# Kernel optimization log

Hardware: AMD Instinct MI355X
Metric: run time of the kernel (lower is better)

The kernel has to match this reference:

```python
import jax, jax.numpy as jnp
import numpy as np

B, NIN, DIN, M, DOUT = 256, 64, 128, 32, 128
SCALE = 1.0 / np.sqrt(DOUT)  # 1/sqrt(out_d_capsules)


def setup_inputs() -> dict:
    key = jax.random.key(0)
    k1, k2, k3 = jax.random.split(key, 3)
    w_const = float(np.sqrt(M / (DIN * NIN)))  # weight_init_const
    return {
        "x": jax.random.normal(k1, (B, NIN, DIN), dtype=jnp.float32),
        "current_act": jax.random.uniform(k2, (B, NIN), dtype=jnp.float32),
        "W": w_const * jax.random.normal(k3, (NIN, DIN, M, DOUT), dtype=jnp.float32),
        "num_iter": 3,
    }


def reference(x, current_act, W, num_iter):
    # Initial pass: next_capsule_value is None -> q0 = softmax(zeros) = 1/M uniform
    # einsum('nm,bna,namd->bmd', q0, x, W) with uniform q0 == mean over m-weighting = /M
    ncv = jnp.einsum('bna,namd->bmd', x, W) / M  # [B, M, Dout]
    q = jnp.full((B, NIN, M), 1.0 / M, dtype=x.dtype)  # query_key from init step
    # Routing iterations (act_type='EM' -> next_act is None; dp=0 -> no dropout)
    for _ in range(max(1, num_iter)):
        logits = jnp.einsum('bna,namd,bmd->bnm', x, W, ncv) * SCALE  # [B, Nin, M]
        q = jax.nn.softmax(logits, axis=2)
        ncv = jnp.einsum('bnm,bna,namd,bn->bmd', q, x, W, current_act)
    # Per-pair votes and routed class embeddings
    votes = jnp.einsum('bna,namd->bnmd', x, W)          # [B, Nin, M, Dout]
    weights = q * current_act[:, :, None]               # [B, Nin, M]
    route_class_emb = weights[..., None] * votes        # [B, Nin, M, Dout]
    return ncv, q, route_class_emb
```

## Files before the change

kernel.cpp:

```cpp
#include <hip/hip_runtime.h>
#include <math.h>

#define B_    256
#define NIN_  64
#define DIN_  128
#define M_    32
#define DOUT_ 128
#define NUM_ITER 3

static constexpr float SCALE = 0.0883883476483184405501f;

typedef __attribute__((ext_vector_type(8))) short bf16x8;
typedef __attribute__((ext_vector_type(4))) float f32x4;

__device__ __forceinline__ unsigned short f2bf(float f) {
    union { float f; unsigned u; } c; c.f = f;
    unsigned r = c.u + 0x7FFFu + ((c.u >> 16) & 1u);
    return (unsigned short)(r >> 16);
}
__device__ __forceinline__ float lo2f(unsigned u) {
    union { unsigned u; float f; } c; c.u = u << 16; return c.f;
}
__device__ __forceinline__ float hi2f(unsigned u) {
    union { unsigned u; float f; } c; c.u = u & 0xffff0000u; return c.f;
}


__global__ __launch_bounds__(256) void k_votes_mfma(const float* __restrict__ x,
                                                    const float* __restrict__ W,
                                                    float* __restrict__ route) {
    const int n    = blockIdx.x;
    const int j0   = blockIdx.y * 512;
    const int t    = threadIdx.x;
    const int w    = t >> 6;
    const int lane = t & 63;
    const int l15  = lane & 15;
    const int l4   = lane >> 4;

    __shared__ __align__(16) char lds[49152];
    char* xbuf = lds;
    char* wbuf = lds + 32768;

    bf16x8 af[4][4];

    for (int h = 0; h < 2; ++h) {
        {
            const int col4 = (t & 15) * 4;
            const int roff = t >> 4;
            const int boff = col4 * 2;
            for (int p = 0; p < 16; ++p) {
                int row = p * 16 + roff;
                const float* src = x + (size_t)row * (NIN_ * DIN_) + (size_t)n * DIN_ + h * 64 + col4;
                float4 v = *(const float4*)src;
                uint2 pk;
                pk.x = (unsigned)f2bf(v.x) | ((unsigned)f2bf(v.y) << 16);
                pk.y = (unsigned)f2bf(v.z) | ((unsigned)f2bf(v.w) << 16);
                *(uint2*)(xbuf + row * 128 + (boff ^ ((row & 7) << 4))) = pk;
            }
        }
        __syncthreads();
#pragma unroll
        for (int mf = 0; mf < 4; ++mf) {
            int row = w * 64 + mf * 16 + l15;
            int sw  = (row & 7) << 4;
#pragma unroll
            for (int kfh = 0; kfh < 2; ++kfh) {
                int kbyte = kfh * 64 + l4 * 16;
                af[mf][h * 2 + kfh] = *(const bf16x8*)(xbuf + row * 128 + (kbyte ^ sw));
            }
        }
        __syncthreads();
    }

    const int jlane = t & 63;
    const int kg    = t >> 6;

    for (int jt = 0; jt < 8; ++jt) {
        {
            const int jcol = j0 + jt * 64 + jlane;
            const float* Wp = W + (size_t)n * (DIN_ * M_ * DOUT_) + jcol;
            const int sw = (jlane & 7) << 4;
#pragma unroll
            for (int c = 0; c < 4; ++c) {
                int kbase = kg * 32 + c * 8;
                unsigned pk[4];
#pragma unroll
                for (int r = 0; r < 4; ++r) {
                    float f0 = __builtin_nontemporal_load(&Wp[(size_t)(kbase + 2 * r)     * 4096]);
                    float f1 = __builtin_nontemporal_load(&Wp[(size_t)(kbase + 2 * r + 1) * 4096]);
                    pk[r] = (unsigned)f2bf(f0) | ((unsigned)f2bf(f1) << 16);
                }
                *(uint4*)(wbuf + jlane * 256 + ((kbase * 2) ^ sw)) = *(uint4*)pk;
            }
        }
        __syncthreads();

        f32x4 acc[4][4];
#pragma unroll
        for (int mf = 0; mf < 4; ++mf)
#pragma unroll
            for (int nf = 0; nf < 4; ++nf) acc[mf][nf] = (f32x4){0.f, 0.f, 0.f, 0.f};

#pragma unroll
        for (int kf = 0; kf < 4; ++kf) {
            bf16x8 bfr[4];
            int kbyte = kf * 64 + l4 * 16;
#pragma unroll
            for (int nf = 0; nf < 4; ++nf) {
                int col = nf * 16 + l15;
                bfr[nf] = *(const bf16x8*)(wbuf + col * 256 + (kbyte ^ ((col & 7) << 4)));
            }
#pragma unroll
            for (int mf = 0; mf < 4; ++mf)
#pragma unroll
                for (int nf = 0; nf < 4; ++nf)
                    acc[mf][nf] = __builtin_amdgcn_mfma_f32_16x16x32_bf16(af[mf][kf], bfr[nf], acc[mf][nf], 0, 0, 0);
        }
        __syncthreads();

#pragma unroll
        for (int mf = 0; mf < 4; ++mf) {
#pragma unroll
            for (int nf = 0; nf < 4; ++nf) {
                const int jb = nf * 16 + l15;
#pragma unroll
                for (int r = 0; r < 4; ++r) {
                    const int b = w * 64 + mf * 16 + l4 * 4 + r;
                    *(unsigned short*)(xbuf + b * 128 + ((jb * 2) ^ ((b & 12) << 3))) = f2bf(acc[mf][nf][r]);
                }
            }
        }
        __syncthreads();

        {
            char* vout = (char*)route;
            const size_t obase = (size_t)524288 + (size_t)n * 8192 + (size_t)(j0 + jt * 64) * 2;
#pragma unroll
            for (int p = 0; p < 8; ++p) {
                const int b = p * 32 + (t >> 3);
                const int c = (t & 7) * 16;
                uint4 val = *(const uint4*)(xbuf + b * 128 + (c ^ ((b & 12) << 3)));
                *(uint4*)(vout + (size_t)b * 1048576 + obase + c) = val;
            }
        }
        __syncthreads();
    }
}

__global__ __launch_bounds__(512, 2) void k_fused(float* __restrict__ route,
                                                  const float* __restrict__ act,
                                                  float* __restrict__ ncv,
                                                  float* __restrict__ q_out) {
    const int b    = blockIdx.x;
    const int t    = threadIdx.x;
    const int base = t * 8;
    const int m    = t >> 4;

    __shared__ float logits_s[8][32];
    __shared__ float w_s[8][32];
    __shared__ float sact[NIN_];
    if (t < 64) sact[t] = act[b * 64 + t];

    const char* vb    = (const char*)route + (size_t)b * 1048576 + 524288;
    const size_t toff = (size_t)t * 16;

    uint4 vA[8], vB[8];
    float ncvp[8], acc[8];

#define LOADC(DST, CC) { \
    _Pragma("unroll") \
    for (int r = 0; r < 8; ++r) \
        DST[r] = *(const uint4*)(vb + (size_t)((CC) * 8 + r) * 8192 + toff); }

#define SUM8(V) { \
    _Pragma("unroll") \
    for (int r = 0; r < 8; ++r) { \
        acc[0] += lo2f(V[r].x); acc[1] += hi2f(V[r].x); \
        acc[2] += lo2f(V[r].y); acc[3] += hi2f(V[r].y); \
        acc[4] += lo2f(V[r].z); acc[5] += hi2f(V[r].z); \
        acc[6] += lo2f(V[r].w); acc[7] += hi2f(V[r].w); } }

#define PH_A(V) { \
    _Pragma("unroll") \
    for (int r = 0; r < 8; ++r) { \
        float p = 0.f; \
        p = fmaf(lo2f(V[r].x), ncvp[0], p); p = fmaf(hi2f(V[r].x), ncvp[1], p); \
        p = fmaf(lo2f(V[r].y), ncvp[2], p); p = fmaf(hi2f(V[r].y), ncvp[3], p); \
        p = fmaf(lo2f(V[r].z), ncvp[4], p); p = fmaf(hi2f(V[r].z), ncvp[5], p); \
        p = fmaf(lo2f(V[r].w), ncvp[6], p); p = fmaf(hi2f(V[r].w), ncvp[7], p); \
        p += __shfl_xor(p, 1); p += __shfl_xor(p, 2); \
        p += __shfl_xor(p, 4); p += __shfl_xor(p, 8); \
        if ((t & 15) == 0) logits_s[r][m] = p * SCALE; \
    } }

#define PH_B(CC, WRF) { \
    if (t < 256) { \
        const int rr = t >> 5; const int ln = t & 31; \
        float l  = logits_s[rr][ln]; \
        float mx = l; \
        mx = fmaxf(mx, __shfl_xor(mx, 1));  mx = fmaxf(mx, __shfl_xor(mx, 2)); \
        mx = fmaxf(mx, __shfl_xor(mx, 4));  mx = fmaxf(mx, __shfl_xor(mx, 8)); \
        mx = fmaxf(mx, __shfl_xor(mx, 16)); \
        float e  = __expf(l - mx); \
        float su = e; \
        su += __shfl_xor(su, 1);  su += __shfl_xor(su, 2); \
        su += __shfl_xor(su, 4);  su += __shfl_xor(su, 8);  su += __shfl_xor(su, 16); \
        float qv = e / su; \
        const int ng = (CC) * 8 + rr; \
        w_s[rr][ln] = qv * sact[ng]; \
        if (WRF) __builtin_nontemporal_store(qv, q_out + (size_t)b * 2048 + (size_t)ng * 32 + ln); \
    } }

#define PH_C(V, CC, WRF) { \
    _Pragma("unroll") \
    for (int r = 0; r < 8; ++r) { \
        const float wg = w_s[r][m]; \
        float f0 = lo2f(V[r].x), f1 = hi2f(V[r].x), f2 = lo2f(V[r].y), f3 = hi2f(V[r].y); \
        float f4 = lo2f(V[r].z), f5 = hi2f(V[r].z), f6 = lo2f(V[r].w), f7 = hi2f(V[r].w); \
        acc[0] = fmaf(wg, f0, acc[0]); acc[1] = fmaf(wg, f1, acc[1]); \
        acc[2] = fmaf(wg, f2, acc[2]); acc[3] = fmaf(wg, f3, acc[3]); \
        acc[4] = fmaf(wg, f4, acc[4]); acc[5] = fmaf(wg, f5, acc[5]); \
        acc[6] = fmaf(wg, f6, acc[6]); acc[7] = fmaf(wg, f7, acc[7]); \
        if (WRF) { \
            f32x4 r0 = {wg * f0, wg * f1, wg * f2, wg * f3}; \
            f32x4 r1 = {wg * f4, wg * f5, wg * f6, wg * f7}; \
            float* rp = route + (size_t)b * 262144 + (size_t)((CC) * 8 + r) * 4096 + base; \
            __builtin_nontemporal_store(r0, (f32x4*)rp); \
            __builtin_nontemporal_store(r1, (f32x4*)(rp + 4)); \
        } \
    } }

#define PROC(V, CC, WRF) { PH_A(V); __syncthreads(); PH_B(CC, WRF); __syncthreads(); PH_C(V, CC, WRF); }

#define ITER_PASS(WRF, WRAP) { \
    _Pragma("unroll") for (int i = 0; i < 8; ++i) acc[i] = 0.f; \
    LOADC(vB, 1); \
    for (int cc = 0; cc < 8; cc += 2) { \
        PROC(vA, cc, WRF); \
        if (cc + 2 < 8) { LOADC(vA, cc + 2); } \
        else if (WRAP)  { LOADC(vA, 0); } \
        PROC(vB, cc + 1, WRF); \
        if (cc + 3 < 8) { LOADC(vB, cc + 3); } \
    } \
    _Pragma("unroll") for (int i = 0; i < 8; ++i) ncvp[i] = acc[i]; }

#pragma unroll
    for (int i = 0; i < 8; ++i) acc[i] = 0.f;
    LOADC(vA, 0);
    LOADC(vB, 1);
    for (int cc = 0; cc < 8; cc += 2) {
        SUM8(vA);
        if (cc + 2 < 8) { LOADC(vA, cc + 2); }
        else            { LOADC(vA, 0); }
        SUM8(vB);
        if (cc + 3 < 8) { LOADC(vB, cc + 3); }
    }
#pragma unroll
    for (int i = 0; i < 8; ++i) ncvp[i] = acc[i] * (1.0f / 32.0f);

    for (int it = 0; it < NUM_ITER - 1; ++it) {
        ITER_PASS(0, 1);
    }
    ITER_PASS(1, 0);

    float* op = ncv + (size_t)b * 4096 + base;
    f32x4 o0 = {ncvp[0], ncvp[1], ncvp[2], ncvp[3]};
    f32x4 o1 = {ncvp[4], ncvp[5], ncvp[6], ncvp[7]};
    __builtin_nontemporal_store(o0, (f32x4*)op);
    __builtin_nontemporal_store(o1, (f32x4*)(op + 4));

#undef LOADC
#undef SUM8
#undef PH_A
#undef PH_B
#undef PH_C
#undef PROC
#undef ITER_PASS
}

extern "C" void kernel_launch(void* const* d_in, const int* in_sizes, int n_in,
                              void* d_out, int out_size, void* d_ws, size_t ws_size,
                              hipStream_t stream) {
    const float* x   = (const float*)d_in[0];
    const float* act = (const float*)d_in[1];
    const float* W   = (const float*)d_in[2];
    (void)in_sizes; (void)n_in; (void)d_ws; (void)ws_size; (void)out_size;

    float* out   = (float*)d_out;
    float* ncv   = out;
    float* q     = out + 1048576;
    float* route = out + 1572864;

    hipLaunchKernelGGL(k_votes_mfma, dim3(64, 8), dim3(256), 0, stream, x, W, route);
    hipLaunchKernelGGL(k_fused, dim3(256), dim3(512), 0, stream, route, act, ncv, q);
}
```

Baseline: 275.9 us.

## Split initial ncv sum into separate kernel and widen fused blocks to 1024 threads

The initial uniform-weighted vote sum now runs in its own kernel that writes ncv to the output buffer. The fused routing kernel reads that ncv back and uses 1024 threads per batch block, each handling 4 output elements instead of 8, with wider shuffle reductions and a manually unrolled chunk loop. Nontemporal stores become plain stores. The goal is more parallelism per batch row and a shorter serial first pass. The cost is an extra launch, more lanes per block stalling at each barrier, and half the bytes in flight per thread.

```diff
diff --git a/kernel.cpp b/kernel.cpp
--- a/kernel.cpp
+++ b/kernel.cpp
@@ -147,14 +147,35 @@
     }
 }
 
-__global__ __launch_bounds__(512, 2) void k_fused(float* __restrict__ route,
-                                                  const float* __restrict__ act,
-                                                  float* __restrict__ ncv,
-                                                  float* __restrict__ q_out) {
+__global__ __launch_bounds__(256) void k_ncv0(const float* __restrict__ route,
+                                              float* __restrict__ ncv) {
+    const int tid = blockIdx.x * 256 + threadIdx.x;
+    const int f   = tid * 8;
+    const int b   = f >> 12;
+    const int r   = f & 4095;
+    const char* vp = (const char*)route + (size_t)b * 1048576 + 524288 + (size_t)r * 2;
+    float s[8] = {0.f, 0.f, 0.f, 0.f, 0.f, 0.f, 0.f, 0.f};
+    for (int n = 0; n < 64; ++n) {
+        uint4 v = *(const uint4*)(vp + (size_t)n * 8192);
+        s[0] += lo2f(v.x); s[1] += hi2f(v.x);
+        s[2] += lo2f(v.y); s[3] += hi2f(v.y);
+        s[4] += lo2f(v.z); s[5] += hi2f(v.z);
+        s[6] += lo2f(v.w); s[7] += hi2f(v.w);
+    }
+    f32x4 o0 = {s[0] * (1.0f/32.0f), s[1] * (1.0f/32.0f), s[2] * (1.0f/32.0f), s[3] * (1.0f/32.0f)};
+    f32x4 o1 = {s[4] * (1.0f/32.0f), s[5] * (1.0f/32.0f), s[6] * (1.0f/32.0f), s[7] * (1.0f/32.0f)};
+    *(f32x4*)(ncv + f)     = o0;
+    *(f32x4*)(ncv + f + 4) = o1;
+}
+
+__global__ __launch_bounds__(1024, 4) void k_fused(float* __restrict__ route,
+                                                   const float* __restrict__ act,
+                                                   float* __restrict__ ncv,
+                                                   float* __restrict__ q_out) {
     const int b    = blockIdx.x;
     const int t    = threadIdx.x;
-    const int base = t * 8;
-    const int m    = t >> 4;
+    const int base = t * 4;
+    const int m    = t >> 5;
 
     __shared__ float logits_s[8][32];
     __shared__ float w_s[8][32];
@@ -162,23 +183,20 @@
     if (t < 64) sact[t] = act[b * 64 + t];
 
     const char* vb    = (const char*)route + (size_t)b * 1048576 + 524288;
-    const size_t toff = (size_t)t * 16;
-
-    uint4 vA[8], vB[8];
-    float ncvp[8], acc[8];
+    const size_t toff = (size_t)t * 8;
+
+    uint2 vA[8], vB[8];
+    float ncvp[4], acc[4];
+
+    {
+        f32x4 n0 = *(const f32x4*)(ncv + (size_t)b * 4096 + base);
+        ncvp[0] = n0.x; ncvp[1] = n0.y; ncvp[2] = n0.z; ncvp[3] = n0.w;
+    }
 
 #define LOADC(DST, CC) { \
     _Pragma("unroll") \
     for (int r = 0; r < 8; ++r) \
-        DST[r] = *(const uint4*)(vb + (size_t)((CC) * 8 + r) * 8192 + toff); }
-
-#define SUM8(V) { \
-    _Pragma("unroll") \
-    for (int r = 0; r < 8; ++r) { \
-        acc[0] += lo2f(V[r].x); acc[1] += hi2f(V[r].x); \
-        acc[2] += lo2f(V[r].y); acc[3] += hi2f(V[r].y); \
-        acc[4] += lo2f(V[r].z); acc[5] += hi2f(V[r].z); \
-        acc[6] += lo2f(V[r].w); acc[7] += hi2f(V[r].w); } }
+        DST[r] = *(const uint2*)(vb + (size_t)((CC) * 8 + r) * 8192 + toff); }
 
 #define PH_A(V) { \
     _Pragma("unroll") \
@@ -186,11 +204,9 @@
         float p = 0.f; \
         p = fmaf(lo2f(V[r].x), ncvp[0], p); p = fmaf(hi2f(V[r].x), ncvp[1], p); \
         p = fmaf(lo2f(V[r].y), ncvp[2], p); p = fmaf(hi2f(V[r].y), ncvp[3], p); \
-        p = fmaf(lo2f(V[r].z), ncvp[4], p); p = fmaf(hi2f(V[r].z), ncvp[5], p); \
-        p = fmaf(lo2f(V[r].w), ncvp[6], p); p = fmaf(hi2f(V[r].w), ncvp[7], p); \
-        p += __shfl_xor(p, 1); p += __shfl_xor(p, 2); \
-        p += __shfl_xor(p, 4); p += __shfl_xor(p, 8); \
-        if ((t & 15) == 0) logits_s[r][m] = p * SCALE; \
+        p += __shfl_xor(p, 1); p += __shfl_xor(p, 2); p += __shfl_xor(p, 4); \
+        p += __shfl_xor(p, 8); p += __shfl_xor(p, 16); \
+        if ((t & 31) == 0) logits_s[r][m] = p * SCALE; \
     } }
 
 #define PH_B(CC, WRF) { \
@@ -208,7 +224,7 @@
         float qv = e / su; \
         const int ng = (CC) * 8 + rr; \
         w_s[rr][ln] = qv * sact[ng]; \
-        if (WRF) __builtin_nontemporal_store(qv, q_out + (size_t)b * 2048 + (size_t)ng * 32 + ln); \
+        if (WRF) q_out[(size_t)b * 2048 + (size_t)ng * 32 + ln] = qv; \
     } }
 
 #define PH_C(V, CC, WRF) { \
@@ -216,61 +232,37 @@
     for (int r = 0; r < 8; ++r) { \
         const float wg = w_s[r][m]; \
         float f0 = lo2f(V[r].x), f1 = hi2f(V[r].x), f2 = lo2f(V[r].y), f3 = hi2f(V[r].y); \
-        float f4 = lo2f(V[r].z), f5 = hi2f(V[r].z), f6 = lo2f(V[r].w), f7 = hi2f(V[r].w); \
         acc[0] = fmaf(wg, f0, acc[0]); acc[1] = fmaf(wg, f1, acc[1]); \
         acc[2] = fmaf(wg, f2, acc[2]); acc[3] = fmaf(wg, f3, acc[3]); \
-        acc[4] = fmaf(wg, f4, acc[4]); acc[5] = fmaf(wg, f5, acc[5]); \
-        acc[6] = fmaf(wg, f6, acc[6]); acc[7] = fmaf(wg, f7, acc[7]); \
         if (WRF) { \
             f32x4 r0 = {wg * f0, wg * f1, wg * f2, wg * f3}; \
-            f32x4 r1 = {wg * f4, wg * f5, wg * f6, wg * f7}; \
-            float* rp = route + (size_t)b * 262144 + (size_t)((CC) * 8 + r) * 4096 + base; \
-            __builtin_nontemporal_store(r0, (f32x4*)rp); \
-            __builtin_nontemporal_store(r1, (f32x4*)(rp + 4)); \
+            *(f32x4*)(route + (size_t)b * 262144 + (size_t)((CC) * 8 + r) * 4096 + base) = r0; \
         } \
     } }
 
 #define PROC(V, CC, WRF) { PH_A(V); __syncthreads(); PH_B(CC, WRF); __syncthreads(); PH_C(V, CC, WRF); }
 
 #define ITER_PASS(WRF, WRAP) { \
-    _Pragma("unroll") for (int i = 0; i < 8; ++i) acc[i] = 0.f; \
+    _Pragma("unroll") for (int i = 0; i < 4; ++i) acc[i] = 0.f; \
     LOADC(vB, 1); \
-    for (int cc = 0; cc < 8; cc += 2) { \
-        PROC(vA, cc, WRF); \
-        if (cc + 2 < 8) { LOADC(vA, cc + 2); } \
-        else if (WRAP)  { LOADC(vA, 0); } \
-        PROC(vB, cc + 1, WRF); \
-        if (cc + 3 < 8) { LOADC(vB, cc + 3); } \
-    } \
-    _Pragma("unroll") for (int i = 0; i < 8; ++i) ncvp[i] = acc[i]; }
-
-#pragma unroll
-    for (int i = 0; i < 8; ++i) acc[i] = 0.f;
+    PROC(vA, 0, WRF); LOADC(vA, 2); \
+    PROC(vB, 1, WRF); LOADC(vB, 3); \
+    PROC(vA, 2, WRF); LOADC(vA, 4); \
+    PROC(vB, 3, WRF); LOADC(vB, 5); \
+    PROC(vA, 4, WRF); LOADC(vA, 6); \
+    PROC(vB, 5, WRF); LOADC(vB, 7); \
+    PROC(vA, 6, WRF); if (WRAP) { LOADC(vA, 0); } \
+    PROC(vB, 7, WRF); \
+    _Pragma("unroll") for (int i = 0; i < 4; ++i) ncvp[i] = acc[i]; }
+
     LOADC(vA, 0);
-    LOADC(vB, 1);
-    for (int cc = 0; cc < 8; cc += 2) {
-        SUM8(vA);
-        if (cc + 2 < 8) { LOADC(vA, cc + 2); }
-        else            { LOADC(vA, 0); }
-        SUM8(vB);
-        if (cc + 3 < 8) { LOADC(vB, cc + 3); }
-    }
-#pragma unroll
-    for (int i = 0; i < 8; ++i) ncvp[i] = acc[i] * (1.0f / 32.0f);
-
-    for (int it = 0; it < NUM_ITER - 1; ++it) {
-        ITER_PASS(0, 1);
-    }
+    ITER_PASS(0, 1);
+    ITER_PASS(0, 1);
     ITER_PASS(1, 0);
 
-    float* op = ncv + (size_t)b * 4096 + base;
-    f32x4 o0 = {ncvp[0], ncvp[1], ncvp[2], ncvp[3]};
-    f32x4 o1 = {ncvp[4], ncvp[5], ncvp[6], ncvp[7]};
-    __builtin_nontemporal_store(o0, (f32x4*)op);
-    __builtin_nontemporal_store(o1, (f32x4*)(op + 4));
+    *(f32x4*)(ncv + (size_t)b * 4096 + base) = (f32x4){ncvp[0], ncvp[1], ncvp[2], ncvp[3]};
 
 #undef LOADC
-#undef SUM8
 #undef PH_A
 #undef PH_B
 #undef PH_C
@@ -292,5 +284,6 @@
     float* route = out + 1572864;
 
     hipLaunchKernelGGL(k_votes_mfma, dim3(64, 8), dim3(256), 0, stream, x, W, route);
-    hipLaunchKernelGGL(k_fused, dim3(256), dim3(512), 0, stream, route, act, ncv, q);
-}
+    hipLaunchKernelGGL(k_ncv0, dim3(512), dim3(256), 0, stream, route, ncv);
+    hipLaunchKernelGGL(k_fused, dim3(256), dim3(1024), 0, stream, route, act, ncv, q);
+}
```

Result: slower. 551.6 us (+99.9%).
